# Kernel tuning notes

Measured on AMD Instinct MI355X. Metric: run time of the kernel, lower is better.

## Reference

```python
import jax, jax.numpy as jnp
import numpy as np
import math

B, S, DM, H, F = 2, 2048, 1024, 16, 192  # F = head_dim init arg; per-head dim = F // 3
DH = F // 3
MAX_BIAS = 8.0


def _get_slopes(n):
    # faithful to ALiBiBias._get_slopes
    def pow2(n):
        start = 2.0 ** (-(2.0 ** (-(math.log2(n) - 3))))
        return [start * start ** i for i in range(n)]
    if math.log2(n).is_integer():
        return pow2(n)
    cp2 = 2 ** math.floor(math.log2(n))
    return pow2(cp2) + _get_slopes(2 * cp2)[0::2][: n - cp2]


def _rope_sin_cos(seq_len, dim):
    inv_freq = 1.0 / (10000.0 ** (jnp.arange(0, dim, 2, dtype=jnp.float32) / dim))
    freqs = jnp.outer(jnp.arange(seq_len, dtype=jnp.float32), inv_freq)  # [S, dim/2]
    # repeat(sin[:,None,:],2,axis=1).reshape(S,-1) == concat([sin,sin],-1)
    sin = jnp.concatenate([jnp.sin(freqs), jnp.sin(freqs)], axis=-1)  # [S, dim]
    cos = jnp.concatenate([jnp.cos(freqs), jnp.cos(freqs)], axis=-1)
    return sin, cos


def _rotate_half(x):
    x1, x2 = jnp.split(x, 2, axis=-1)
    return jnp.concatenate([-x2, x1], axis=-1)


def setup_inputs() -> dict:
    key = jax.random.key(0)
    kx, kq, ko = jax.random.split(key, 3)
    x = jax.random.normal(kx, (B, S, DM), dtype=jnp.float32)
    w_qkv = jax.random.normal(kq, (DM, H, F), dtype=jnp.float32) * (1.0 / math.sqrt(DM))
    b_qkv = jnp.zeros((H, F), dtype=jnp.float32)
    w_out = jax.random.normal(ko, (H, DH, DM), dtype=jnp.float32) * (1.0 / math.sqrt(H * DH))
    b_out = jnp.zeros((DM,), dtype=jnp.float32)
    return {"x": x, "w_qkv": w_qkv, "b_qkv": b_qkv, "w_out": w_out, "b_out": b_out}


def reference(x, w_qkv, b_qkv, w_out, b_out):
    b, s, dm = x.shape
    h, f = w_qkv.shape[1], w_qkv.shape[2]
    dh = f // 3
    # fused QKV projection: [B,S,H,F], then 3-way split on the feature axis
    qkv = jnp.einsum('bsd,dhf->bshf', x, w_qkv) + b_qkv
    q, k, v = jnp.split(qkv, 3, axis=-1)  # each [B,S,H,DH]
    # RoPE (rotate_half convention), broadcast over heads
    sin, cos = _rope_sin_cos(s, dh)
    sin, cos = sin[:, None, :], cos[:, None, :]  # [S,1,DH]
    q = q * cos + _rotate_half(q) * sin
    k = k * cos + _rotate_half(k) * sin
    # [B,H,S,DH]
    q = q.transpose(0, 2, 1, 3)
    k = k.transpose(0, 2, 1, 3)
    v = v.transpose(0, 2, 1, 3)
    # scores scaled by sqrt(head_dim init arg), as in the original non-flash path
    scores = jnp.einsum('bhqd,bhkd->bhqk', q, k) / jnp.sqrt(jnp.float32(f))
    # ALiBi bias
    slopes = jnp.asarray(_get_slopes(h), dtype=jnp.float32)  # [H]
    pos = jnp.arange(s, dtype=jnp.float32)
    rel = pos[None, :] - pos[:, None]  # j - i
    rel = jnp.where(rel > 0, 0.0, rel)
    alibi = rel[None, :, :] * slopes[:, None, None] * MAX_BIAS  # [H,S,S]
    scores = scores + alibi[None]  # [B,H,S,S]
    # causal mask
    causal = jnp.tril(jnp.ones((s, s), dtype=jnp.float32))
    scores = jnp.where(causal == 0, -1e9, scores)
    weights = jax.nn.softmax(scores, axis=-1)
    attn = jnp.einsum('bhqk,bhkd->bhqd', weights, v).transpose(0, 2, 1, 3)  # [B,S,H,DH]
    return jnp.einsum('bshd,hdm->bsm', attn, w_out) + b_out
```

## Files before the change

### kernel.cpp

```cpp
#include <hip/hip_runtime.h>
#include <math.h>

static constexpr int B_  = 2;
static constexpr int S_  = 2048;
static constexpr int H_  = 16;
static constexpr int DH_ = 64;
static constexpr float QSCALE2_ = 0.104117589f;
static constexpr float C8L2_    = 11.5415603f;

typedef __attribute__((ext_vector_type(8))) short short8;
typedef __attribute__((ext_vector_type(4))) float floatx4;

__device__ __forceinline__ float bf2f(unsigned short u) {
    union { unsigned int i; float f; } c; c.i = ((unsigned int)u) << 16; return c.f;
}
__device__ __forceinline__ unsigned short f2bf(float f) {
    union { float f; unsigned int i; } c; c.f = f;
    unsigned int x = c.i;
    unsigned int r = (x + 0x7fffu + ((x >> 16) & 1u)) >> 16;
    if ((x & 0x7f800000u) == 0x7f800000u) r = x >> 16;
    return (unsigned short)r;
}
__device__ __forceinline__ void load_lds16(const unsigned short* g, unsigned short* l) {
    __builtin_amdgcn_global_load_lds(
        (const __attribute__((address_space(1))) unsigned int*)g,
        (__attribute__((address_space(3))) unsigned int*)l, 16, 0, 0);
}

__global__ __launch_bounds__(256) void prep(
    const float* __restrict__ x,     unsigned short* __restrict__ xb,
    const float* __restrict__ w_qkv, unsigned short* __restrict__ wqkvT,
    const float* __restrict__ w_out, unsigned short* __restrict__ woutT)
{
    __shared__ float t[32][33];
    const int bid = blockIdx.x;
    if (bid < 4096) {
        const int i = bid * 256 + threadIdx.x;
        const float4 v = reinterpret_cast<const float4*>(x)[i];
        ushort4 r;
        r.x = f2bf(v.x); r.y = f2bf(v.y); r.z = f2bf(v.z); r.w = f2bf(v.w);
        reinterpret_cast<ushort4*>(xb)[i] = r;
        return;
    }
    const float* in; unsigned short* out; int NN, bx, by;
    if (bid < 7168) {
        in = w_qkv; out = wqkvT; NN = 3072;
        const int b2 = bid - 4096; bx = b2 % 96; by = b2 / 96;
    } else {
        in = w_out; out = woutT; NN = 1024;
        const int b2 = bid - 7168; bx = b2 & 31; by = b2 >> 5;
    }
    const int n0 = bx * 32;
    const int k0 = by * 32;
    const int tn = threadIdx.x & 31, tk = threadIdx.x >> 5;
    #pragma unroll
    for (int i = 0; i < 4; ++i)
        t[tk + 8 * i][tn] = in[(size_t)(k0 + tk + 8 * i) * NN + n0 + tn];
    __syncthreads();
    #pragma unroll
    for (int i = 0; i < 4; ++i)
        out[(size_t)(n0 + tk + 8 * i) * 1024 + k0 + tn] = f2bf(t[tn][tk + 8 * i]);
}

__global__ __launch_bounds__(256) void gemm_qkv(
    const unsigned short* __restrict__ A, const unsigned short* __restrict__ BT,
    const float* __restrict__ bias,
    unsigned short* __restrict__ O0, unsigned short* __restrict__ O1,
    unsigned short* __restrict__ O2)
{
    __shared__ unsigned short As[128 * 32];
    __shared__ unsigned short Bs[128 * 32];

    const int tid  = threadIdx.x;
    const int wave = tid >> 6;
    const int lane = tid & 63;
    const int quad = lane >> 4;
    const int lm   = lane & 15;
    const int wm = (wave >> 1) * 64;
    const int wn = (wave & 1) * 64;
    const int n0 = blockIdx.x * 128;
    const int m0 = blockIdx.y * 128;

    floatx4 acc[4][4] = {};

    const int sr = lane >> 2;
    const int sc = lane & 3;

    for (int k0 = 0; k0 < 1024; k0 += 32) {
        #pragma unroll
        for (int rep = 0; rep < 2; ++rep) {
            const int r = wave * 32 + rep * 16;
            load_lds16(A  + (size_t)(m0 + r + sr) * 1024 + k0 + sc * 8, &As[r * 32]);
            load_lds16(BT + (size_t)(n0 + r + sr) * 1024 + k0 + sc * 8, &Bs[r * 32]);
        }
        __syncthreads();
        short8 af[4], bf[4];
        #pragma unroll
        for (int i = 0; i < 4; ++i) {
            af[i] = *reinterpret_cast<const short8*>(&As[(wm + i * 16 + lm) * 32 + quad * 8]);
            bf[i] = *reinterpret_cast<const short8*>(&Bs[(wn + i * 16 + lm) * 32 + quad * 8]);
        }
        #pragma unroll
        for (int mi = 0; mi < 4; ++mi)
            #pragma unroll
            for (int ni = 0; ni < 4; ++ni)
                acc[mi][ni] = __builtin_amdgcn_mfma_f32_16x16x32_bf16(
                    af[mi], bf[ni], acc[mi][ni], 0, 0, 0);
        __syncthreads();
    }

    const int nbase = n0 + wn;
    const int h   = nbase / 192;
    const int sec = (nbase - h * 192) >> 6;
    float bia[4];
    #pragma unroll
    for (int ni = 0; ni < 4; ++ni) bia[ni] = bias[nbase + ni * 16 + lm];
    unsigned short* Out = (sec == 0) ? O0 : ((sec == 1) ? O1 : O2);

    if (sec == 2) {
        #pragma unroll
        for (int mi = 0; mi < 4; ++mi) {
            const int m  = m0 + wm + mi * 16 + quad * 4;
            const int bb = m >> 11;
            const int s  = m & (S_ - 1);
            const size_t rowb = (size_t)(bb * H_ + h) * DH_;
            #pragma unroll
            for (int ni = 0; ni < 4; ++ni) {
                const int d = ni * 16 + lm;
                ushort4 w;
                w.x = f2bf(acc[mi][ni][0] + bia[ni]);
                w.y = f2bf(acc[mi][ni][1] + bia[ni]);
                w.z = f2bf(acc[mi][ni][2] + bia[ni]);
                w.w = f2bf(acc[mi][ni][3] + bia[ni]);
                *reinterpret_cast<ushort4*>(&Out[(rowb + d) * S_ + s]) = w;
            }
        }
    } else {
        const float qscale = (sec == 0) ? QSCALE2_ : 1.0f;
        const float nlf = -13.287712379549449f / 32.0f;
        const float invf0 = exp2f((float)lm * nlf);
        const float invf1 = exp2f((float)(lm + 16) * nlf);
        #pragma unroll
        for (int mi = 0; mi < 4; ++mi) {
            #pragma unroll
            for (int r = 0; r < 4; ++r) {
                const int m  = m0 + wm + mi * 16 + quad * 4 + r;
                const int bb = m >> 11;
                const int s  = m & (S_ - 1);
                const size_t obase = ((size_t)(bb * H_ + h) * S_ + s) * DH_;
                const float a0 = (float)s * invf0, a1 = (float)s * invf1;
                const float sn0 = __sinf(a0), cs0 = __cosf(a0);
                const float sn1 = __sinf(a1), cs1 = __cosf(a1);
                #pragma unroll
                for (int ni = 0; ni < 4; ++ni) {
                    const int d = ni * 16 + lm;
                    const float v = acc[mi][ni][r]     + bia[ni];
                    const float p = acc[mi][ni ^ 2][r] + bia[ni ^ 2];
                    const float cs = (ni & 1) ? cs1 : cs0;
                    const float sn = (ni & 1) ? sn1 : sn0;
                    float res = (d < 32) ? (v * cs - p * sn) : (v * cs + p * sn);
                    Out[obase + d] = f2bf(res * qscale);
                }
            }
        }
    }
}

__global__ __launch_bounds__(256) void gemm_out(
    const unsigned short* __restrict__ A, const unsigned short* __restrict__ BT,
    const float* __restrict__ bias, float* __restrict__ Of)
{
    __shared__ unsigned short As[64 * 32];
    __shared__ unsigned short Bs[128 * 32];

    const int tid  = threadIdx.x;
    const int wave = tid >> 6;
    const int lane = tid & 63;
    const int quad = lane >> 4;
    const int lm   = lane & 15;
    const int wm = (wave >> 1) * 32;
    const int wn = (wave & 1) * 64;
    const int n0 = blockIdx.x * 128;
    const int m0 = blockIdx.y * 64;

    floatx4 acc[2][4] = {};

    const int sr = lane >> 2;
    const int sc = lane & 3;

    for (int k0 = 0; k0 < 1024; k0 += 32) {
        load_lds16(A + (size_t)(m0 + wave * 16 + sr) * 1024 + k0 + sc * 8,
                   &As[wave * 16 * 32]);
        #pragma unroll
        for (int rep = 0; rep < 2; ++rep) {
            const int r = wave * 32 + rep * 16;
            load_lds16(BT + (size_t)(n0 + r + sr) * 1024 + k0 + sc * 8, &Bs[r * 32]);
        }
        __syncthreads();
        short8 af[2], bf[4];
        #pragma unroll
        for (int i = 0; i < 2; ++i)
            af[i] = *reinterpret_cast<const short8*>(&As[(wm + i * 16 + lm) * 32 + quad * 8]);
        #pragma unroll
        for (int i = 0; i < 4; ++i)
            bf[i] = *reinterpret_cast<const short8*>(&Bs[(wn + i * 16 + lm) * 32 + quad * 8]);
        #pragma unroll
        for (int mi = 0; mi < 2; ++mi)
            #pragma unroll
            for (int ni = 0; ni < 4; ++ni)
                acc[mi][ni] = __builtin_amdgcn_mfma_f32_16x16x32_bf16(
                    af[mi], bf[ni], acc[mi][ni], 0, 0, 0);
        __syncthreads();
    }

    #pragma unroll
    for (int ni = 0; ni < 4; ++ni) {
        const int gn = n0 + wn + ni * 16 + lm;
        const float b = bias[gn];
        #pragma unroll
        for (int mi = 0; mi < 2; ++mi) {
            const int gm = m0 + wm + mi * 16 + quad * 4;
            #pragma unroll
            for (int r = 0; r < 4; ++r)
                Of[(size_t)(gm + r) * 1024 + gn] = acc[mi][ni][r] + b;
        }
    }
}

__global__ __launch_bounds__(256, 4) void flash_mfma(
    const unsigned short* __restrict__ Q, const unsigned short* __restrict__ K,
    const unsigned short* __restrict__ VT, unsigned short* __restrict__ Ao)
{
    __shared__ unsigned short Ks[2][64 * 64];
    __shared__ unsigned short VTs[2][64 * 64];
    __shared__ unsigned short Ps[4][16 * 64];

    const int bi = blockIdx.x;
    const int qt = 31 - (bi >> 5);
    const int bh = bi & 31;
    const int h  = bh & 15;
    const int b  = bh >> 4;
    const int tid  = threadIdx.x;
    const int wave = tid >> 6;
    const int lane = tid & 63;
    const int quad = lane >> 4;
    const int lm   = lane & 15;
    const int srow = tid >> 2;
    const int sc8  = tid & 3;

    const int swa = (sc8)     ^ (srow & 7);
    const int swb = (sc8 + 4) ^ (srow & 7);
    const int rq0 = (quad)     ^ (lm & 7);
    const int rq1 = (quad + 4) ^ (lm & 7);

    const unsigned short* Kg  = K  + (size_t)bh * S_ * DH_;
    const unsigned short* VTg = VT + (size_t)bh * DH_ * S_;

    const float slope2 = exp2f(-0.5f * (float)(h + 1)) * (8.0f * 1.44269504f);
    const float d64 = 64.0f * slope2;

    int   koff[4];
    float alb[4];
    #pragma unroll
    for (int t = 0; t < 4; ++t) {
        koff[t] = t * 16 + quad * 4 - wave * 16 - lm;
        alb[t]  = (float)koff[t] * slope2 - C8L2_;
    }

    unsigned short* Pw = &Ps[wave][0];
    int pwr[4];
    #pragma unroll
    for (int t = 0; t < 4; ++t)
        pwr[t] = lm * 64 + ((2 * t + (quad >> 1)) ^ (lm & 7)) * 8 + (quad & 1) * 4;

    const unsigned short* Qrow =
        Q + ((size_t)bh * S_ + (size_t)(qt * 64 + wave * 16 + lm)) * DH_;
    const short8 aq0 = *reinterpret_cast<const short8*>(Qrow + quad * 8);
    const short8 aq1 = *reinterpret_cast<const short8*>(Qrow + 32 + quad * 8);

    float crk[4];
    #pragma unroll
    for (int r = 0; r < 4; ++r)
        crk[r] = (float)r * slope2 - (float)qt * d64;

    float l_one = 0.0f;
    floatx4 acc_o[4] = {};

    short8 ka, kb, va, vb;
    {
        const unsigned short* kr = Kg + (size_t)srow * DH_ + sc8 * 8;
        ka = *reinterpret_cast<const short8*>(kr);
        kb = *reinterpret_cast<const short8*>(kr + 32);
        const unsigned short* vr = VTg + (size_t)srow * S_ + sc8 * 8;
        va = *reinterpret_cast<const short8*>(vr);
        vb = *reinterpret_cast<const short8*>(vr + 32);
    }
    *reinterpret_cast<short8*>(&Ks[0][srow * 64 + swa * 8])  = ka;
    *reinterpret_cast<short8*>(&Ks[0][srow * 64 + swb * 8])  = kb;
    *reinterpret_cast<short8*>(&VTs[0][srow * 64 + swa * 8]) = va;
    *reinterpret_cast<short8*>(&VTs[0][srow * 64 + swb * 8]) = vb;
    if (qt > 0) {
        const unsigned short* kr = Kg + (size_t)(64 + srow) * DH_ + sc8 * 8;
        ka = *reinterpret_cast<const short8*>(kr);
        kb = *reinterpret_cast<const short8*>(kr + 32);
        const unsigned short* vr = VTg + (size_t)srow * S_ + 64 + sc8 * 8;
        va = *reinterpret_cast<const short8*>(vr);
        vb = *reinterpret_cast<const short8*>(vr + 32);
    }
    __syncthreads();

    for (int kt = 0; kt <= qt; ++kt) {
        const int cur = kt & 1;

        if (kt < qt) {
            const int nxt = cur ^ 1;
            *reinterpret_cast<short8*>(&Ks[nxt][srow * 64 + swa * 8])  = ka;
            *reinterpret_cast<short8*>(&Ks[nxt][srow * 64 + swb * 8])  = kb;
            *reinterpret_cast<short8*>(&VTs[nxt][srow * 64 + swa * 8]) = va;
            *reinterpret_cast<short8*>(&VTs[nxt][srow * 64 + swb * 8]) = vb;
            if (kt + 1 < qt) {
                const unsigned short* kr =
                    Kg + (size_t)((kt + 2) * 64 + srow) * DH_ + sc8 * 8;
                ka = *reinterpret_cast<const short8*>(kr);
                kb = *reinterpret_cast<const short8*>(kr + 32);
                const unsigned short* vr =
                    VTg + (size_t)srow * S_ + (kt + 2) * 64 + sc8 * 8;
                va = *reinterpret_cast<const short8*>(vr);
                vb = *reinterpret_cast<const short8*>(vr + 32);
            }
        }

        floatx4 sacc[4] = {};
        __builtin_amdgcn_s_setprio(1);
        #pragma unroll
        for (int t = 0; t < 4; ++t) {
            const short8 k0 = *reinterpret_cast<const short8*>(&Ks[cur][(t * 16 + lm) * 64 + rq0 * 8]);
            const short8 k1 = *reinterpret_cast<const short8*>(&Ks[cur][(t * 16 + lm) * 64 + rq1 * 8]);
            sacc[t] = __builtin_amdgcn_mfma_f32_16x16x32_bf16(k0, aq0, sacc[t], 0, 0, 0);
            sacc[t] = __builtin_amdgcn_mfma_f32_16x16x32_bf16(k1, aq1, sacc[t], 0, 0, 0);
        }
        __builtin_amdgcn_s_setprio(0);

        const bool diag = (kt == qt);
        #pragma unroll
        for (int t = 0; t < 4; ++t) {
            float pv[4];
            #pragma unroll
            for (int r = 0; r < 4; ++r) {
                const float x = (sacc[t][r] + alb[t]) + crk[r];
                float e;
                asm("v_exp_f32 %0, %1" : "=v"(e) : "v"(x));
                if (diag && (koff[t] + r) > 0) e = 0.0f;
                pv[r] = e;
            }
            l_one += (pv[0] + pv[1]) + (pv[2] + pv[3]);
            unsigned int lo, hi;
            asm("v_cvt_pk_bf16_f32 %0, %1, %2" : "=v"(lo) : "v"(pv[0]), "v"(pv[1]));
            asm("v_cvt_pk_bf16_f32 %0, %1, %2" : "=v"(hi) : "v"(pv[2]), "v"(pv[3]));
            uint2 w; w.x = lo; w.y = hi;
            *reinterpret_cast<uint2*>(&Pw[pwr[t]]) = w;
        }
        #pragma unroll
        for (int r = 0; r < 4; ++r) crk[r] += d64;

        const short8 ap0 = *reinterpret_cast<const short8*>(&Pw[lm * 64 + rq0 * 8]);
        const short8 ap1 = *reinterpret_cast<const short8*>(&Pw[lm * 64 + rq1 * 8]);
        __builtin_amdgcn_s_setprio(1);
        #pragma unroll
        for (int t = 0; t < 4; ++t) {
            const short8 v0 = *reinterpret_cast<const short8*>(&VTs[cur][(t * 16 + lm) * 64 + rq0 * 8]);
            const short8 v1 = *reinterpret_cast<const short8*>(&VTs[cur][(t * 16 + lm) * 64 + rq1 * 8]);
            acc_o[t] = __builtin_amdgcn_mfma_f32_16x16x32_bf16(ap0, v0, acc_o[t], 0, 0, 0);
            acc_o[t] = __builtin_amdgcn_mfma_f32_16x16x32_bf16(ap1, v1, acc_o[t], 0, 0, 0);
        }
        __builtin_amdgcn_s_setprio(0);
        __syncthreads();
    }

    l_one += __shfl_xor(l_one, 16);
    l_one += __shfl_xor(l_one, 32);
    #pragma unroll
    for (int r = 0; r < 4; ++r) {
        const float lr = __shfl(l_one, quad * 4 + r);
        const float inv_l = 1.0f / lr;
        const int s = qt * 64 + wave * 16 + quad * 4 + r;
        const size_t obase = ((size_t)(b * S_ + s) * H_ + h) * DH_;
        #pragma unroll
        for (int t = 0; t < 4; ++t)
            Ao[obase + t * 16 + lm] = f2bf(acc_o[t][r] * inv_l);
    }
}

extern "C" void kernel_launch(void* const* d_in, const int* in_sizes, int n_in,
                              void* d_out, int out_size, void* d_ws, size_t ws_size,
                              hipStream_t stream)
{
    const float *x = nullptr, *w_qkv = nullptr, *b_qkv = nullptr,
                *w_out = nullptr, *b_out = nullptr;
    for (int i = 0; i < n_in; ++i) {
        switch (in_sizes[i]) {
            case 4194304: x     = (const float*)d_in[i]; break;
            case 3145728: w_qkv = (const float*)d_in[i]; break;
            case 3072:    b_qkv = (const float*)d_in[i]; break;
            case 1048576: w_out = (const float*)d_in[i]; break;
            case 1024:    b_out = (const float*)d_in[i]; break;
        }
    }
    if (!x)     x     = (const float*)d_in[0];
    if (!w_qkv) w_qkv = (const float*)d_in[1];
    if (!b_qkv) b_qkv = (const float*)d_in[2];
    if (!w_out) w_out = (const float*)d_in[3];
    if (!b_out) b_out = (const float*)d_in[4];

    float* out = (float*)d_out;
    unsigned short* ws16 = (unsigned short*)d_ws;

    unsigned short* xb     = ws16;
    unsigned short* wqkvT  = ws16 + (size_t)4194304;
    unsigned short* woutT  = ws16 + (size_t)7340032;
    unsigned short* Qb     = ws16 + (size_t)8388608;
    unsigned short* Kb     = ws16 + (size_t)12582912;
    unsigned short* Vb     = ws16 + (size_t)16777216;
    unsigned short* Aob    = ws16 + (size_t)20971520;

    prep<<<8192, 256, 0, stream>>>(x, xb, w_qkv, wqkvT, w_out, woutT);

    gemm_qkv<<<dim3(24, 32), 256, 0, stream>>>(
        xb, wqkvT, b_qkv, Qb, Kb, Vb);
    flash_mfma<<<dim3(1024), 256, 0, stream>>>(Qb, Kb, Vb, Aob);
    gemm_out<<<dim3(8, 64), 256, 0, stream>>>(Aob, woutT, b_out, out);
}
```

Measured before the change: 174.7 us.

## Rewrite QKV GEMM with 256x256 tiles, double-buffered LDS and swizzled layout

```diff
diff --git a/kernel.cpp b/kernel.cpp
--- a/kernel.cpp
+++ b/kernel.cpp
@@ -62,54 +62,129 @@
         out[(size_t)(n0 + tk + 8 * i) * 1024 + k0 + tn] = f2bf(t[tn][tk + 8 * i]);
 }
 
-__global__ __launch_bounds__(256) void gemm_qkv(
+__global__ __launch_bounds__(512, 2) void gemm_qkv(
     const unsigned short* __restrict__ A, const unsigned short* __restrict__ BT,
     const float* __restrict__ bias,
     unsigned short* __restrict__ O0, unsigned short* __restrict__ O1,
     unsigned short* __restrict__ O2)
 {
-    __shared__ unsigned short As[128 * 32];
-    __shared__ unsigned short Bs[128 * 32];
+    __shared__ unsigned short As[2][256 * 64];
+    __shared__ unsigned short Bs[2][256 * 64];
 
     const int tid  = threadIdx.x;
     const int wave = tid >> 6;
     const int lane = tid & 63;
     const int quad = lane >> 4;
     const int lm   = lane & 15;
-    const int wm = (wave >> 1) * 64;
-    const int wn = (wave & 1) * 64;
-    const int n0 = blockIdx.x * 128;
-    const int m0 = blockIdx.y * 128;
-
-    floatx4 acc[4][4] = {};
-
-    const int sr = lane >> 2;
-    const int sc = lane & 3;
-
-    for (int k0 = 0; k0 < 1024; k0 += 32) {
-        #pragma unroll
-        for (int rep = 0; rep < 2; ++rep) {
-            const int r = wave * 32 + rep * 16;
-            load_lds16(A  + (size_t)(m0 + r + sr) * 1024 + k0 + sc * 8, &As[r * 32]);
-            load_lds16(BT + (size_t)(n0 + r + sr) * 1024 + k0 + sc * 8, &Bs[r * 32]);
-        }
-        __syncthreads();
-        short8 af[4], bf[4];
-        #pragma unroll
-        for (int i = 0; i < 4; ++i) {
-            af[i] = *reinterpret_cast<const short8*>(&As[(wm + i * 16 + lm) * 32 + quad * 8]);
-            bf[i] = *reinterpret_cast<const short8*>(&Bs[(wn + i * 16 + lm) * 32 + quad * 8]);
-        }
-        #pragma unroll
-        for (int mi = 0; mi < 4; ++mi)
+    const int wr   = wave >> 2;
+    const int wc   = wave & 3;
+    const int n0 = blockIdx.x * 256;
+    const int m0 = blockIdx.y * 256;
+    const int lr = lane >> 3;
+    const int swz8 = ((lane & 7) ^ lr) * 8;
+    const int l7 = lm & 7;
+
+    floatx4 acc[8][4] = {};
+
+    auto stage_half = [&](int sb, int T, int h) {
+        const int isB = h >> 1;
+        const int r0  = (h & 1) * 128 + wave * 16;
+        #pragma unroll
+        for (int c = 0; c < 2; ++c) {
+            const int row = r0 + c * 8;
+            if (!isB)
+                load_lds16(A + (size_t)(m0 + row + lr) * 1024 + T * 64 + swz8,
+                           &As[sb][row * 64]);
+            else
+                load_lds16(BT + (size_t)(n0 + row + lr) * 1024 + T * 64 + swz8,
+                           &Bs[sb][row * 64]);
+        }
+    };
+
+    #pragma unroll
+    for (int h = 0; h < 4; ++h) stage_half(0, 0, h);
+
+    #pragma unroll 1
+    for (int i = 0; i < 8; ++i) {
+        #pragma unroll
+        for (int g = 0; g < 2; ++g) {
+            const int rb = g;
+            const int sb = g ^ 1;
+            const int st = 2 * i + 1 + g;
+            const bool doSt = (st <= 15);
+
+            asm volatile("s_waitcnt vmcnt(0)" ::: "memory");
+            __builtin_amdgcn_s_barrier();
+
+            short8 bf0[4], bf1[4], af[4];
+
+            if (doSt) stage_half(sb, st, 0);
             #pragma unroll
             for (int ni = 0; ni < 4; ++ni)
-                acc[mi][ni] = __builtin_amdgcn_mfma_f32_16x16x32_bf16(
-                    af[mi], bf[ni], acc[mi][ni], 0, 0, 0);
-        __syncthreads();
-    }
-
-    const int nbase = n0 + wn;
+                bf0[ni] = *reinterpret_cast<const short8*>(
+                    &Bs[rb][(wc * 64 + ni * 16 + lm) * 64 + (quad ^ l7) * 8]);
+            #pragma unroll
+            for (int t = 0; t < 4; ++t)
+                af[t] = *reinterpret_cast<const short8*>(
+                    &As[rb][(wr * 128 + t * 16 + lm) * 64 + (quad ^ l7) * 8]);
+            __builtin_amdgcn_s_setprio(1);
+            #pragma unroll
+            for (int t = 0; t < 4; ++t)
+                #pragma unroll
+                for (int ni = 0; ni < 4; ++ni)
+                    acc[t][ni] = __builtin_amdgcn_mfma_f32_16x16x32_bf16(
+                        af[t], bf0[ni], acc[t][ni], 0, 0, 0);
+            __builtin_amdgcn_s_setprio(0);
+
+            if (doSt) stage_half(sb, st, 1);
+            #pragma unroll
+            for (int ni = 0; ni < 4; ++ni)
+                bf1[ni] = *reinterpret_cast<const short8*>(
+                    &Bs[rb][(wc * 64 + ni * 16 + lm) * 64 + ((4 + quad) ^ l7) * 8]);
+            #pragma unroll
+            for (int t = 0; t < 4; ++t)
+                af[t] = *reinterpret_cast<const short8*>(
+                    &As[rb][(wr * 128 + t * 16 + lm) * 64 + ((4 + quad) ^ l7) * 8]);
+            __builtin_amdgcn_s_setprio(1);
+            #pragma unroll
+            for (int t = 0; t < 4; ++t)
+                #pragma unroll
+                for (int ni = 0; ni < 4; ++ni)
+                    acc[t][ni] = __builtin_amdgcn_mfma_f32_16x16x32_bf16(
+                        af[t], bf1[ni], acc[t][ni], 0, 0, 0);
+            __builtin_amdgcn_s_setprio(0);
+
+            if (doSt) stage_half(sb, st, 2);
+            #pragma unroll
+            for (int t = 0; t < 4; ++t)
+                af[t] = *reinterpret_cast<const short8*>(
+                    &As[rb][(wr * 128 + 64 + t * 16 + lm) * 64 + (quad ^ l7) * 8]);
+            __builtin_amdgcn_s_setprio(1);
+            #pragma unroll
+            for (int t = 0; t < 4; ++t)
+                #pragma unroll
+                for (int ni = 0; ni < 4; ++ni)
+                    acc[4 + t][ni] = __builtin_amdgcn_mfma_f32_16x16x32_bf16(
+                        af[t], bf0[ni], acc[4 + t][ni], 0, 0, 0);
+            __builtin_amdgcn_s_setprio(0);
+
+            if (doSt) stage_half(sb, st, 3);
+            #pragma unroll
+            for (int t = 0; t < 4; ++t)
+                af[t] = *reinterpret_cast<const short8*>(
+                    &As[rb][(wr * 128 + 64 + t * 16 + lm) * 64 + ((4 + quad) ^ l7) * 8]);
+            __builtin_amdgcn_s_setprio(1);
+            #pragma unroll
+            for (int t = 0; t < 4; ++t)
+                #pragma unroll
+                for (int ni = 0; ni < 4; ++ni)
+                    acc[4 + t][ni] = __builtin_amdgcn_mfma_f32_16x16x32_bf16(
+                        af[t], bf1[ni], acc[4 + t][ni], 0, 0, 0);
+            __builtin_amdgcn_s_setprio(0);
+        }
+    }
+
+    const int nbase = n0 + wc * 64;
     const int h   = nbase / 192;
     const int sec = (nbase - h * 192) >> 6;
     float bia[4];
@@ -119,8 +194,8 @@
 
     if (sec == 2) {
         #pragma unroll
-        for (int mi = 0; mi < 4; ++mi) {
-            const int m  = m0 + wm + mi * 16 + quad * 4;
+        for (int mi = 0; mi < 8; ++mi) {
+            const int m  = m0 + wr * 128 + mi * 16 + quad * 4;
             const int bb = m >> 11;
             const int s  = m & (S_ - 1);
             const size_t rowb = (size_t)(bb * H_ + h) * DH_;
@@ -141,10 +216,10 @@
         const float invf0 = exp2f((float)lm * nlf);
         const float invf1 = exp2f((float)(lm + 16) * nlf);
         #pragma unroll
-        for (int mi = 0; mi < 4; ++mi) {
+        for (int mi = 0; mi < 8; ++mi) {
             #pragma unroll
             for (int r = 0; r < 4; ++r) {
-                const int m  = m0 + wm + mi * 16 + quad * 4 + r;
+                const int m  = m0 + wr * 128 + mi * 16 + quad * 4 + r;
                 const int bb = m >> 11;
                 const int s  = m & (S_ - 1);
                 const size_t obase = ((size_t)(bb * H_ + h) * S_ + s) * DH_;
@@ -425,7 +500,7 @@
 
     prep<<<8192, 256, 0, stream>>>(x, xb, w_qkv, wqkvT, w_out, woutT);
 
-    gemm_qkv<<<dim3(24, 32), 256, 0, stream>>>(
+    gemm_qkv<<<dim3(12, 16), 512, 0, stream>>>(
         xb, wqkvT, b_qkv, Qb, Kb, Vb);
     flash_mfma<<<dim3(1024), 256, 0, stream>>>(Qb, Kb, Vb, Aob);
     gemm_out<<<dim3(8, 64), 256, 0, stream>>>(Aob, woutT, b_out, out);
```

After: 177.8 us. About the same (+1.8%).

## Enlarge QKV GEMM tiles to 256x256 with multi-buffered async LDS pipeline

Applied to the files above, without the earlier changes.

```diff
diff --git a/kernel.cpp b/kernel.cpp
--- a/kernel.cpp
+++ b/kernel.cpp
@@ -62,54 +62,81 @@
         out[(size_t)(n0 + tk + 8 * i) * 1024 + k0 + tn] = f2bf(t[tn][tk + 8 * i]);
 }
 
-__global__ __launch_bounds__(256) void gemm_qkv(
+__global__ __launch_bounds__(512, 2) void gemm_qkv(
     const unsigned short* __restrict__ A, const unsigned short* __restrict__ BT,
     const float* __restrict__ bias,
     unsigned short* __restrict__ O0, unsigned short* __restrict__ O1,
     unsigned short* __restrict__ O2)
 {
-    __shared__ unsigned short As[128 * 32];
-    __shared__ unsigned short Bs[128 * 32];
+    __shared__ unsigned short As[4][256 * 32];
+    __shared__ unsigned short Bs[4][256 * 32];
 
     const int tid  = threadIdx.x;
     const int wave = tid >> 6;
     const int lane = tid & 63;
     const int quad = lane >> 4;
     const int lm   = lane & 15;
-    const int wm = (wave >> 1) * 64;
-    const int wn = (wave & 1) * 64;
-    const int n0 = blockIdx.x * 128;
-    const int m0 = blockIdx.y * 128;
-
-    floatx4 acc[4][4] = {};
-
-    const int sr = lane >> 2;
-    const int sc = lane & 3;
-
-    for (int k0 = 0; k0 < 1024; k0 += 32) {
-        #pragma unroll
-        for (int rep = 0; rep < 2; ++rep) {
-            const int r = wave * 32 + rep * 16;
-            load_lds16(A  + (size_t)(m0 + r + sr) * 1024 + k0 + sc * 8, &As[r * 32]);
-            load_lds16(BT + (size_t)(n0 + r + sr) * 1024 + k0 + sc * 8, &Bs[r * 32]);
-        }
-        __syncthreads();
-        short8 af[4], bf[4];
-        #pragma unroll
-        for (int i = 0; i < 4; ++i) {
-            af[i] = *reinterpret_cast<const short8*>(&As[(wm + i * 16 + lm) * 32 + quad * 8]);
-            bf[i] = *reinterpret_cast<const short8*>(&Bs[(wn + i * 16 + lm) * 32 + quad * 8]);
-        }
-        #pragma unroll
-        for (int mi = 0; mi < 4; ++mi)
+    const int wr   = wave >> 2;
+    const int wc   = wave & 3;
+    const int n0 = blockIdx.x * 256;
+    const int m0 = blockIdx.y * 256;
+
+    const int srow   = tid >> 2;
+    const int scs    = ((tid & 3) ^ (srow & 3)) * 8;
+    const int rchunk = (quad ^ (lm & 3)) * 8;
+
+    floatx4 acc[8][4] = {};
+
+    for (int T = 0; T < 2; ++T) {
+        const int buf = T;
+        #pragma unroll
+        for (int i = 0; i < 2; ++i) {
+            const int r = i * 128 + srow;
+            load_lds16(A  + (size_t)(m0 + r) * 1024 + T * 32 + scs,
+                       &As[buf][(i * 128 + wave * 16) * 32]);
+            load_lds16(BT + (size_t)(n0 + r) * 1024 + T * 32 + scs,
+                       &Bs[buf][(i * 128 + wave * 16) * 32]);
+        }
+    }
+
+    #pragma unroll 1
+    for (int t = 0; t < 32; ++t) {
+        if (t == 31) asm volatile("s_waitcnt vmcnt(0)" ::: "memory");
+        else         asm volatile("s_waitcnt vmcnt(4)" ::: "memory");
+        __builtin_amdgcn_s_barrier();
+
+        if (t + 2 < 32) {
+            const int T = t + 2, buf = T & 3;
+            #pragma unroll
+            for (int i = 0; i < 2; ++i) {
+                const int r = i * 128 + srow;
+                load_lds16(A  + (size_t)(m0 + r) * 1024 + T * 32 + scs,
+                           &As[buf][(i * 128 + wave * 16) * 32]);
+                load_lds16(BT + (size_t)(n0 + r) * 1024 + T * 32 + scs,
+                           &Bs[buf][(i * 128 + wave * 16) * 32]);
+            }
+        }
+
+        const int rb = t & 3;
+        short8 bf[4];
+        #pragma unroll
+        for (int ni = 0; ni < 4; ++ni)
+            bf[ni] = *reinterpret_cast<const short8*>(
+                &Bs[rb][(wc * 64 + ni * 16 + lm) * 32 + rchunk]);
+        __builtin_amdgcn_s_setprio(1);
+        #pragma unroll
+        for (int mi = 0; mi < 8; ++mi) {
+            const short8 af = *reinterpret_cast<const short8*>(
+                &As[rb][(wr * 128 + mi * 16 + lm) * 32 + rchunk]);
             #pragma unroll
             for (int ni = 0; ni < 4; ++ni)
                 acc[mi][ni] = __builtin_amdgcn_mfma_f32_16x16x32_bf16(
-                    af[mi], bf[ni], acc[mi][ni], 0, 0, 0);
-        __syncthreads();
-    }
-
-    const int nbase = n0 + wn;
+                    af, bf[ni], acc[mi][ni], 0, 0, 0);
+        }
+        __builtin_amdgcn_s_setprio(0);
+    }
+
+    const int nbase = n0 + wc * 64;
     const int h   = nbase / 192;
     const int sec = (nbase - h * 192) >> 6;
     float bia[4];
@@ -119,8 +146,8 @@
 
     if (sec == 2) {
         #pragma unroll
-        for (int mi = 0; mi < 4; ++mi) {
-            const int m  = m0 + wm + mi * 16 + quad * 4;
+        for (int mi = 0; mi < 8; ++mi) {
+            const int m  = m0 + wr * 128 + mi * 16 + quad * 4;
             const int bb = m >> 11;
             const int s  = m & (S_ - 1);
             const size_t rowb = (size_t)(bb * H_ + h) * DH_;
@@ -141,10 +168,10 @@
         const float invf0 = exp2f((float)lm * nlf);
         const float invf1 = exp2f((float)(lm + 16) * nlf);
         #pragma unroll
-        for (int mi = 0; mi < 4; ++mi) {
+        for (int mi = 0; mi < 8; ++mi) {
             #pragma unroll
             for (int r = 0; r < 4; ++r) {
-                const int m  = m0 + wm + mi * 16 + quad * 4 + r;
+                const int m  = m0 + wr * 128 + mi * 16 + quad * 4 + r;
                 const int bb = m >> 11;
                 const int s  = m & (S_ - 1);
                 const size_t obase = ((size_t)(bb * H_ + h) * S_ + s) * DH_;
@@ -425,7 +452,7 @@
 
     prep<<<8192, 256, 0, stream>>>(x, xb, w_qkv, wqkvT, w_out, woutT);
 
-    gemm_qkv<<<dim3(24, 32), 256, 0, stream>>>(
+    gemm_qkv<<<dim3(12, 16), 512, 0, stream>>>(
         xb, wqkvT, b_qkv, Qb, Kb, Vb);
     flash_mfma<<<dim3(1024), 256, 0, stream>>>(Qb, Kb, Vb, Aob);
     gemm_out<<<dim3(8, 64), 256, 0, stream>>>(Aob, woutT, b_out, out);
```

New measurement: 188.2 us. 7.7% more time.
